# Optimization experiments

Hardware: AMD Instinct MI355X
Metric: run time of the kernel (lower is better)

Reference implementation:

```python
import jax, jax.numpy as jnp
import numpy as np

DIM = 256
NUM_HEADS = 8
HEAD_DIM = DIM // NUM_HEADS  # 32 (MQA: k/v projected to a single head)
RPE_DIM = 128
P = 10            # cpb table resolution per axis ('bilinear_4_10')
MAX_VALUE = 4.0
LOG_SCALE = 512.0
LOG2_8 = 3.0      # np.log2(8)


def _trilinear_sample(table, grid):
    """torch F.grid_sample 3D, mode='bilinear', padding_mode='zeros', align_corners=True.
    table: [C, D, H, W]; grid: [M, 3] with (x,y,z) in [-1,1] -> returns [C, M]."""
    C, D, H, W = table.shape
    x = (grid[:, 0] + 1.0) * 0.5 * (W - 1)
    y = (grid[:, 1] + 1.0) * 0.5 * (H - 1)
    z = (grid[:, 2] + 1.0) * 0.5 * (D - 1)
    x0f, y0f, z0f = jnp.floor(x), jnp.floor(y), jnp.floor(z)
    wx1, wy1, wz1 = x - x0f, y - y0f, z - z0f
    wx0, wy0, wz0 = 1.0 - wx1, 1.0 - wy1, 1.0 - wz1
    x0 = x0f.astype(jnp.int32); x1 = x0 + 1
    y0 = y0f.astype(jnp.int32); y1 = y0 + 1
    z0 = z0f.astype(jnp.int32); z1 = z0 + 1

    def corner(iz, iy, ix, w):
        inb = (iz >= 0) & (iz < D) & (iy >= 0) & (iy < H) & (ix >= 0) & (ix < W)
        v = table[:, jnp.clip(iz, 0, D - 1), jnp.clip(iy, 0, H - 1), jnp.clip(ix, 0, W - 1)]
        return v * jnp.where(inb, w, 0.0)[None, :]

    return (corner(z0, y0, x0, wz0 * wy0 * wx0) + corner(z0, y0, x1, wz0 * wy0 * wx1)
          + corner(z0, y1, x0, wz0 * wy1 * wx0) + corner(z0, y1, x1, wz0 * wy1 * wx1)
          + corner(z1, y0, x0, wz1 * wy0 * wx0) + corner(z1, y0, x1, wz1 * wy0 * wx1)
          + corner(z1, y1, x0, wz1 * wy1 * wx0) + corner(z1, y1, x1, wz1 * wy1 * wx1))


def setup_inputs() -> dict:
    rng = jax.random.key(0)
    ks = jax.random.split(rng, 12)
    B, nQ, nK = 2, 256, 2048
    s = 0.02
    return {
        "query": jax.random.normal(ks[0], (nQ, B, DIM), jnp.float32),
        "key": jax.random.normal(ks[1], (nK, B, DIM), jnp.float32),
        "reference_point": jax.random.normal(ks[2], (B, nQ, 8, 3), jnp.float32),
        "reference_angle": jax.random.normal(ks[3], (B, nQ), jnp.float32),
        "xyz_vol": jax.random.normal(ks[4], (B, nK, 3), jnp.float32),
        "q_w": jax.random.normal(ks[5], (DIM, DIM), jnp.float32) * s,
        "q_b": jnp.zeros((DIM,), jnp.float32),
        "k_w": jax.random.normal(ks[6], (DIM, HEAD_DIM), jnp.float32) * s,
        "k_b": jnp.zeros((HEAD_DIM,), jnp.float32),
        "v_w": jax.random.normal(ks[7], (DIM, HEAD_DIM), jnp.float32) * s,
        "v_b": jnp.zeros((HEAD_DIM,), jnp.float32),
        "proj_w": jax.random.normal(ks[8], (DIM, DIM), jnp.float32) * s,
        "proj_b": jnp.zeros((DIM,), jnp.float32),
        "cpb_w1": jax.random.normal(ks[9], (8, 3, RPE_DIM), jnp.float32) * s,
        "cpb_b1": jnp.zeros((8, RPE_DIM), jnp.float32),
        "cpb_w2": jax.random.normal(ks[10], (8, RPE_DIM, NUM_HEADS), jnp.float32) * s,
    }


def reference(query, key, reference_point, reference_angle, xyz_vol,
              q_w, q_b, k_w, k_b, v_w, v_b, proj_w, proj_b,
              cpb_w1, cpb_b1, cpb_w2):
    B, nQ = reference_point.shape[:2]
    nK = xyz_vol.shape[1]
    q_in = jnp.transpose(query, (1, 0, 2))  # [B, nQ, DIM]
    k_in = jnp.transpose(key, (1, 0, 2))    # [B, nK, DIM]

    # CPB MLP evaluated on the fixed coords table -> per-corner tables [8, NUM_HEADS, P, P, P]
    lin = jnp.linspace(-MAX_VALUE, MAX_VALUE, P, dtype=jnp.float32)
    coords = jnp.stack(jnp.meshgrid(lin, lin, lin, indexing='ij'), axis=-1)  # [P,P,P,3]
    hid = jax.nn.relu(jnp.einsum('pqrc,icd->ipqrd', coords, cpb_w1) + cpb_b1[:, None, None, None, :])
    tables = jnp.einsum('ipqrd,idh->ihpqr', hid, cpb_w2)

    # log-scaled relative deltas for all 8 corners (angle_type=='' -> no rotation branch)
    d = reference_point[:, :, None, :, :] - xyz_vol[:, None, :, None, :]  # [B,nQ,nK,8,3]
    d = jnp.sign(d) * jnp.log2(jnp.abs(d) * LOG_SCALE + 1.0) / LOG2_8 / MAX_VALUE
    grids = jnp.moveaxis(d, 3, 0).reshape(8, -1, 3)  # [8, B*nQ*nK, 3]

    sampled = jax.vmap(_trilinear_sample)(tables, grids)  # [8, NUM_HEADS, M]
    rpe = jnp.transpose(sampled.sum(0).reshape(NUM_HEADS, B, nQ, nK), (1, 0, 2, 3))  # [B,H,nQ,nK]

    scale = HEAD_DIM ** -0.5
    q = (q_in @ q_w + q_b).reshape(B, nQ, NUM_HEADS, HEAD_DIM)
    k = k_in @ k_w + k_b  # [B, nK, HEAD_DIM] (single shared KV head)
    v = k_in @ v_w + v_b
    attn = jnp.einsum('bqhd,bkd->bhqk', q * scale, k) + rpe
    attn = jax.nn.softmax(attn, axis=-1)
    x = jnp.einsum('bhqk,bkd->bqhd', attn, v).reshape(B, nQ, DIM)
    x = x @ proj_w + proj_b
    return jnp.transpose(x, (1, 0, 2)), attn
```

## Files before the change

kernel.cpp:

```cpp
#include <hip/hip_runtime.h>
#include <hip/hip_bf16.h>
#include <cstdint>

#define NQ 256
#define NK 2048
#define BB 2
#define SCALE 0.17677669529663687f

#define TB_OFF 0u
#define QP_OFF 128000u
#define KT_OFF 652288u
#define VP_OFF 1176576u

typedef unsigned short u16;
typedef _Float16 h16;
union U16x8 { uint4 u; h16 h[8]; };

__global__ __launch_bounds__(512) void k_prep(const float* __restrict__ query,
                                              const float* __restrict__ key,
                                              const float* __restrict__ qw,
                                              const float* __restrict__ qb,
                                              const float* __restrict__ kw,
                                              const float* __restrict__ kb,
                                              const float* __restrict__ vw,
                                              const float* __restrict__ vb,
                                              const float* __restrict__ w1g,
                                              const float* __restrict__ b1g,
                                              const float* __restrict__ w2g,
                                              u16* __restrict__ tb,
                                              float* __restrict__ qp,
                                              float* __restrict__ kpT,
                                              float* __restrict__ vp) {
  __shared__ __align__(16) char smraw[16 * 257 * 4];
  int bid = blockIdx.x, t = threadIdx.x;

  if (bid < 256) {
    float (*rows)[257] = (float(*)[257])smraw;
    int b = bid >> 7, kc = bid & 127;
    for (int idx = t; idx < 4096; idx += 512) {
      int r = idx >> 8, m = idx & 255;
      rows[r][m] = key[((kc * 16 + r) * BB + b) * 256 + m];
    }
    __syncthreads();
    int ks = t >> 5, d = t & 31;
    float a = kb[d], av = vb[d];
    #pragma unroll 4
    for (int m = 0; m < 256; ++m) {
      float rv = rows[ks][m];
      a  = fmaf(rv, kw[m * 32 + d], a);
      av = fmaf(rv, vw[m * 32 + d], av);
    }
    int k = kc * 16 + ks;
    vp[(b * NK + k) * 32 + d] = av;
    __syncthreads();
    float* f1 = (float*)smraw;
    f1[d * 16 + ks] = a;
    __syncthreads();
    int dd = t >> 4, kk = t & 15;
    kpT[(b * 32 + dd) * NK + kc * 16 + kk] = f1[dd * 16 + kk];
  } else if (bid < 320) {
    float (*rows)[257] = (float(*)[257])smraw;
    int qg = bid - 256;
    for (int idx = t; idx < 2048; idx += 512) {
      int r = idx >> 8, m = idx & 255;
      int g = qg * 8 + r, b = g >> 8, q = g & 255;
      rows[r][m] = query[(q * BB + b) * 256 + m];
    }
    __syncthreads();
    int r = t >> 6, c0 = (t & 63) * 4;
    int g = qg * 8 + r;
    float4 acc = *(const float4*)&qb[c0];
    #pragma unroll 4
    for (int m = 0; m < 256; ++m) {
      float rv = rows[r][m];
      float4 w4 = *(const float4*)&qw[m * 256 + c0];
      acc.x = fmaf(rv, w4.x, acc.x); acc.y = fmaf(rv, w4.y, acc.y);
      acc.z = fmaf(rv, w4.z, acc.z); acc.w = fmaf(rv, w4.w, acc.w);
    }
    float4 o; o.x = acc.x * SCALE; o.y = acc.y * SCALE; o.z = acc.z * SCALE; o.w = acc.w * SCALE;
    *(float4*)&qp[g * 256 + c0] = o;
  } else {
    float* w1 = (float*)smraw;
    float* b1 = w1 + 384;
    float* w2 = b1 + 128;
    int ib = bid - 320;
    int i = ib >> 2, cc = ib & 3;
    for (int idx = t; idx < 384; idx += 512) w1[idx] = w1g[i * 384 + idx];
    if (t < 128) b1[t] = b1g[i * 128 + t];
    for (int idx = t; idx < 1024; idx += 512) w2[idx] = w2g[i * 1024 + idx];
    __syncthreads();
    if (t < 250) {
      int cell = cc * 250 + t;
      int z = cell / 100, y = (cell / 10) % 10, x = cell % 10;
      const float step = 8.0f / 9.0f;
      float cz = -4.f + z * step, cy = -4.f + y * step, cx = -4.f + x * step;
      float o0 = 0, o1 = 0, o2 = 0, o3 = 0, o4 = 0, o5 = 0, o6 = 0, o7 = 0;
      for (int d = 0; d < 128; ++d) {
        float h = fmaxf(fmaf(cz, w1[d], fmaf(cy, w1[128 + d], fmaf(cx, w1[256 + d], b1[d]))), 0.f);
        const float* w2r = &w2[d * 8];
        o0 = fmaf(h, w2r[0], o0); o1 = fmaf(h, w2r[1], o1);
        o2 = fmaf(h, w2r[2], o2); o3 = fmaf(h, w2r[3], o3);
        o4 = fmaf(h, w2r[4], o4); o5 = fmaf(h, w2r[5], o5);
        o6 = fmaf(h, w2r[6], o6); o7 = fmaf(h, w2r[7], o7);
      }
      U16x8 R;
      R.h[0] = (h16)o0; R.h[1] = (h16)o1; R.h[2] = (h16)o2; R.h[3] = (h16)o3;
      R.h[4] = (h16)o4; R.h[5] = (h16)o5; R.h[6] = (h16)o6; R.h[7] = (h16)o7;
      *(uint4*)&tb[i * 8000 + cell * 8] = R.u;
    }
  }
}

struct Axis { int o0, o1; float w0, w1; };

static __device__ __forceinline__ Axis axis_setup(float dv, int stride) {
  float g = copysignf(__log2f(fmaf(fabsf(dv), 512.f, 1.f)) * (1.f / 12.f), dv);
  float p = fmaf(g, 4.5f, 4.5f);
  float f = floorf(p);
  int i0 = (int)f;
  float w1v = p - f;
  float w0v = 1.f - w1v;
  Axis a;
  a.w0 = ((unsigned)i0 <= 9u) ? w0v : 0.f;
  a.w1 = ((unsigned)(i0 + 1) <= 9u) ? w1v : 0.f;
  int c0 = min(max(i0, 0), 9);
  int c1 = min(max(i0 + 1, 0), 9);
  a.o0 = c0 * stride;
  a.o1 = c1 * stride;
  return a;
}

#define MIX2(A0, A1, U32, W) \
  asm("v_fma_mix_f32 %0, %1, %2, %0 op_sel:[0,0,0] op_sel_hi:[1,0,0]" : "+v"(A0) : "v"(U32), "v"(W)); \
  asm("v_fma_mix_f32 %0, %1, %2, %0 op_sel:[1,0,0] op_sel_hi:[1,0,0]" : "+v"(A1) : "v"(U32), "v"(W));

#define DO_CORNER(U, W, J) do { float ww = (W); \
  MIX2(acc[0][J], acc[1][J], (U).x, ww) \
  MIX2(acc[2][J], acc[3][J], (U).y, ww) \
  MIX2(acc[4][J], acc[5][J], (U).z, ww) \
  MIX2(acc[6][J], acc[7][J], (U).w, ww) } while (0)

__global__ __launch_bounds__(1024, 4) void k_mega(const u16* __restrict__ tbw,
                                                  const float* __restrict__ qp,
                                                  const float* __restrict__ kpT,
                                                  const float* __restrict__ xyz,
                                                  const float* __restrict__ refp,
                                                  const float* __restrict__ vp,
                                                  const float* __restrict__ pw,
                                                  const float* __restrict__ pb,
                                                  float* __restrict__ attn,
                                                  float* __restrict__ out) {
  __shared__ __align__(16) char un[131072];
  __shared__ __align__(16) float red4[2][8][8][32];
  __shared__ __align__(16) float qrow[2][256];
  __shared__ __align__(16) float rp[2][24];
  __shared__ __align__(16) float red[2][64];
  u16* tb = (u16*)un;
  float* p = (float*)un;

  int t = threadIdx.x;
  int b = blockIdx.x >> 7, qc = blockIdx.x & 127;
  for (int idx = t; idx < 8000; idx += 1024)
    ((uint4*)tb)[idx] = ((const uint4*)tbw)[idx];
  if (t < 128) {
    int qh2 = t >> 6, c = t & 63;
    ((float4*)qrow[qh2])[c] = ((const float4*)(qp + (b * 256 + qc * 2 + qh2) * 256))[c];
  } else if (t < 140) {
    int idx = t - 128;
    int qh2 = idx / 6, c = idx % 6;
    ((float4*)rp[qh2])[c] = ((const float4*)(refp + (b * 256 + qc * 2 + qh2) * 24))[c];
  }
  __syncthreads();

  int wv = t >> 6, l = t & 63;
  int qh = wv >> 3, wvl = wv & 7;
  int q = qc * 2 + qh;
  int k0 = wvl * 256 + l * 4;
  float acc[8][4] = {};

  const float* kT = kpT + b * (32 * NK);
  #pragma unroll 2
  for (int dq = 0; dq < 8; ++dq) {
    const float* kp0 = kT + (dq * 4) * NK + k0;
    float4 kv0 = *(const float4*)(kp0);
    float4 kv1 = *(const float4*)(kp0 + NK);
    float4 kv2 = *(const float4*)(kp0 + 2 * NK);
    float4 kv3 = *(const float4*)(kp0 + 3 * NK);
    #pragma unroll
    for (int h = 0; h < 8; ++h) {
      float4 qv = *(const float4*)&qrow[qh][h * 32 + dq * 4];
      acc[h][0] = fmaf(qv.x, kv0.x, fmaf(qv.y, kv1.x, fmaf(qv.z, kv2.x, fmaf(qv.w, kv3.x, acc[h][0]))));
      acc[h][1] = fmaf(qv.x, kv0.y, fmaf(qv.y, kv1.y, fmaf(qv.z, kv2.y, fmaf(qv.w, kv3.y, acc[h][1]))));
      acc[h][2] = fmaf(qv.x, kv0.z, fmaf(qv.y, kv1.z, fmaf(qv.z, kv2.z, fmaf(qv.w, kv3.z, acc[h][2]))));
      acc[h][3] = fmaf(qv.x, kv0.w, fmaf(qv.y, kv1.w, fmaf(qv.z, kv2.w, fmaf(qv.w, kv3.w, acc[h][3]))));
    }
  }

  {
    const float* xp = xyz + (size_t)(b * NK + k0) * 3;
    float4 X0 = *(const float4*)(xp);
    float4 X1 = *(const float4*)(xp + 4);
    float4 X2 = *(const float4*)(xp + 8);
    float xv[4] = { X0.x, X0.w, X1.z, X2.y };
    float yv[4] = { X0.y, X1.x, X1.w, X2.z };
    float zv[4] = { X0.z, X1.y, X2.x, X2.w };
    #pragma unroll 1
    for (int i = 0; i < 8; ++i) {
      float rx = rp[qh][i * 3 + 0];
      float ry = rp[qh][i * 3 + 1];
      float rz = rp[qh][i * 3 + 2];
      const u16* tp = tb + i * 8000;
      #pragma unroll
      for (int j = 0; j < 4; ++j) {
        Axis ax = axis_setup(rx - xv[j], 8);
        Axis ay = axis_setup(ry - yv[j], 80);
        Axis az = axis_setup(rz - zv[j], 800);
        int o00 = az.o0 + ay.o0, o01 = az.o0 + ay.o1;
        int o10 = az.o1 + ay.o0, o11 = az.o1 + ay.o1;
        float w00 = az.w0 * ay.w0, w01 = az.w0 * ay.w1;
        float w10 = az.w1 * ay.w0, w11 = az.w1 * ay.w1;
        uint4 u;
        u = *(const uint4*)(tp + o00 + ax.o0); DO_CORNER(u, w00 * ax.w0, j);
        u = *(const uint4*)(tp + o00 + ax.o1); DO_CORNER(u, w00 * ax.w1, j);
        u = *(const uint4*)(tp + o01 + ax.o0); DO_CORNER(u, w01 * ax.w0, j);
        u = *(const uint4*)(tp + o01 + ax.o1); DO_CORNER(u, w01 * ax.w1, j);
        u = *(const uint4*)(tp + o10 + ax.o0); DO_CORNER(u, w10 * ax.w0, j);
        u = *(const uint4*)(tp + o10 + ax.o1); DO_CORNER(u, w10 * ax.w1, j);
        u = *(const uint4*)(tp + o11 + ax.o0); DO_CORNER(u, w11 * ax.w0, j);
        u = *(const uint4*)(tp + o11 + ax.o1); DO_CORNER(u, w11 * ax.w1, j);
      }
    }
  }

  float mx[8];
  #pragma unroll
  for (int h = 0; h < 8; ++h) {
    float m = fmaxf(fmaxf(acc[h][0], acc[h][1]), fmaxf(acc[h][2], acc[h][3]));
    #pragma unroll
    for (int off = 32; off >= 1; off >>= 1) m = fmaxf(m, __shfl_xor(m, off, 64));
    mx[h] = m;
  }
  if (l == 0) {
    #pragma unroll
    for (int h = 0; h < 8; ++h) red[qh][h * 8 + wvl] = mx[h];
  }
  __syncthreads();
  #pragma unroll
  for (int h = 0; h < 8; ++h) {
    float4 r0 = *(const float4*)&red[qh][h * 8];
    float4 r1 = *(const float4*)&red[qh][h * 8 + 4];
    mx[h] = fmaxf(fmaxf(fmaxf(r0.x, r0.y), fmaxf(r0.z, r0.w)),
                  fmaxf(fmaxf(r1.x, r1.y), fmaxf(r1.z, r1.w)));
  }
  __syncthreads();
  float sm[8];
  #pragma unroll
  for (int h = 0; h < 8; ++h) {
    acc[h][0] = __expf(acc[h][0] - mx[h]);
    acc[h][1] = __expf(acc[h][1] - mx[h]);
    acc[h][2] = __expf(acc[h][2] - mx[h]);
    acc[h][3] = __expf(acc[h][3] - mx[h]);
    float s = (acc[h][0] + acc[h][1]) + (acc[h][2] + acc[h][3]);
    #pragma unroll
    for (int off = 32; off >= 1; off >>= 1) s += __shfl_xor(s, off, 64);
    sm[h] = s;
  }
  if (l == 0) {
    #pragma unroll
    for (int h = 0; h < 8; ++h) red[qh][h * 8 + wvl] = sm[h];
  }
  __syncthreads();
  #pragma unroll
  for (int h = 0; h < 8; ++h) {
    float4 r0 = *(const float4*)&red[qh][h * 8];
    float4 r1 = *(const float4*)&red[qh][h * 8 + 4];
    float s = ((r0.x + r0.y) + (r0.z + r0.w)) + ((r1.x + r1.y) + (r1.z + r1.w));
    float inv = 1.f / s;
    float4 pv;
    pv.x = acc[h][0] * inv; pv.y = acc[h][1] * inv;
    pv.z = acc[h][2] * inv; pv.w = acc[h][3] * inv;
    *(float4*)&p[(qh * 8 + h) * 2048 + k0] = pv;
    *(float4*)&attn[((size_t)((b * 8 + h) * 256 + q)) * 2048 + k0] = pv;
  }
  __syncthreads();

  {
    int ch = wv >> 1, pqh = wv & 1;
    int ks2 = l >> 3, dq = l & 7;
    float a2[8][4] = {};
    const float* vbase = vp + ((size_t)(b * NK + ch * 256)) * 32 + dq * 4;
    const float* prow = p + pqh * 16384 + ch * 256;
    #pragma unroll 2
    for (int kk = 0; kk < 32; ++kk) {
      int ko = kk * 8 + ks2;
      float4 v4 = *(const float4*)&vbase[ko * 32];
      #pragma unroll
      for (int h = 0; h < 8; ++h) {
        float pvv = prow[h * 2048 + ko];
        a2[h][0] = fmaf(pvv, v4.x, a2[h][0]);
        a2[h][1] = fmaf(pvv, v4.y, a2[h][1]);
        a2[h][2] = fmaf(pvv, v4.z, a2[h][2]);
        a2[h][3] = fmaf(pvv, v4.w, a2[h][3]);
      }
    }
    #pragma unroll
    for (int off = 8; off <= 32; off <<= 1) {
      #pragma unroll
      for (int h = 0; h < 8; ++h) {
        a2[h][0] += __shfl_xor(a2[h][0], off, 64);
        a2[h][1] += __shfl_xor(a2[h][1], off, 64);
        a2[h][2] += __shfl_xor(a2[h][2], off, 64);
        a2[h][3] += __shfl_xor(a2[h][3], off, 64);
      }
    }
    if (ks2 == 0) {
      #pragma unroll
      for (int h = 0; h < 8; ++h) {
        float4 w4; w4.x = a2[h][0]; w4.y = a2[h][1]; w4.z = a2[h][2]; w4.w = a2[h][3];
        *(float4*)&red4[pqh][ch][h][dq * 4] = w4;
      }
    }
  }
  __syncthreads();
  if (t < 512) {
    int pqh = t >> 8, m = t & 255;
    int h = m >> 5, d = m & 31;
    float s = 0.f;
    #pragma unroll
    for (int ch = 0; ch < 8; ++ch) s += red4[pqh][ch][h][d];
    qrow[pqh][m] = s;
  }
  __syncthreads();

  {
    float* scratch = (float*)red4;
    int c = t & 255, half = (t >> 8) & 1, pqh = t >> 9;
    int m0 = half * 128;
    float a = 0.f;
    #pragma unroll 4
    for (int m = 0; m < 128; ++m) {
      a = fmaf(qrow[pqh][m0 + m], pw[(m0 + m) * 256 + c], a);
    }
    scratch[(pqh * 2 + half) * 256 + c] = a;
  }
  __syncthreads();
  if (t < 512) {
    float* scratch = (float*)red4;
    int pqh = t >> 8, c = t & 255;
    float v = scratch[(pqh * 2) * 256 + c] + scratch[(pqh * 2 + 1) * 256 + c] + pb[c];
    int qq = qc * 2 + pqh;
    out[(qq * BB + b) * 256 + c] = v;
  }
}

extern "C" void kernel_launch(void* const* d_in, const int* in_sizes, int n_in,
                              void* d_out, int out_size, void* d_ws, size_t ws_size,
                              hipStream_t stream) {
  const float* query = (const float*)d_in[0];
  const float* key   = (const float*)d_in[1];
  const float* refp  = (const float*)d_in[2];
  const float* xyz   = (const float*)d_in[4];
  const float* qw    = (const float*)d_in[5];
  const float* qb    = (const float*)d_in[6];
  const float* kw    = (const float*)d_in[7];
  const float* kb    = (const float*)d_in[8];
  const float* vw    = (const float*)d_in[9];
  const float* vb    = (const float*)d_in[10];
  const float* pw    = (const float*)d_in[11];
  const float* pb    = (const float*)d_in[12];
  const float* w1    = (const float*)d_in[13];
  const float* b1    = (const float*)d_in[14];
  const float* w2    = (const float*)d_in[15];

  char* ws = (char*)d_ws;
  u16*   tb  = (u16*)(ws + TB_OFF);
  float* qp  = (float*)(ws + QP_OFF);
  float* kpT = (float*)(ws + KT_OFF);
  float* vp  = (float*)(ws + VP_OFF);
  float* out  = (float*)d_out;
  float* attn = out + 131072;

  hipLaunchKernelGGL(k_prep, dim3(352), dim3(512),  0, stream,
                     query, key, qw, qb, kw, kb, vw, vb, w1, b1, w2, tb, qp, kpT, vp);
  hipLaunchKernelGGL(k_mega, dim3(256), dim3(1024), 0, stream,
                     tb, qp, kpT, xyz, refp, vp, pw, pb, attn, out);
}
```

Before: 185.4 us.

## Split mega kernel to one query per block with two-pass table staging

Each block now handles one query instead of two, and the grid doubles to 512 blocks to fill more CUs. Shared memory is halved to 64KB, so the 8 CPB tables are loaded into LDS in two passes of four with extra barriers. Attention stores are coalesced through LDS, and the PV and projection stages are rebalanced to the single query. The cost is a second table load per block and more total table traffic, in exchange for better CU occupancy and parallelism.

```diff
diff --git a/kernel.cpp b/kernel.cpp
--- a/kernel.cpp
+++ b/kernel.cpp
@@ -140,7 +140,7 @@
   MIX2(acc[4][J], acc[5][J], (U).z, ww) \
   MIX2(acc[6][J], acc[7][J], (U).w, ww) } while (0)
 
-__global__ __launch_bounds__(1024, 4) void k_mega(const u16* __restrict__ tbw,
+__global__ __launch_bounds__(1024, 8) void k_mega(const u16* __restrict__ tbw,
                                                   const float* __restrict__ qp,
                                                   const float* __restrict__ kpT,
                                                   const float* __restrict__ xyz,
@@ -150,84 +150,82 @@
                                                   const float* __restrict__ pb,
                                                   float* __restrict__ attn,
                                                   float* __restrict__ out) {
-  __shared__ __align__(16) char un[131072];
-  __shared__ __align__(16) float red4[2][8][8][32];
-  __shared__ __align__(16) float qrow[2][256];
-  __shared__ __align__(16) float rp[2][24];
-  __shared__ __align__(16) float red[2][64];
+  __shared__ __align__(16) char un[65536];
+  __shared__ __align__(16) float red4[4][8][32];
+  __shared__ __align__(16) float qrow[256];
+  __shared__ __align__(16) float rp[24];
+  __shared__ __align__(16) float red[128];
   u16* tb = (u16*)un;
   float* p = (float*)un;
 
   int t = threadIdx.x;
-  int b = blockIdx.x >> 7, qc = blockIdx.x & 127;
-  for (int idx = t; idx < 8000; idx += 1024)
+  int b = blockIdx.x >> 8, q = blockIdx.x & 255;
+
+  for (int idx = t; idx < 4000; idx += 1024)
     ((uint4*)tb)[idx] = ((const uint4*)tbw)[idx];
-  if (t < 128) {
-    int qh2 = t >> 6, c = t & 63;
-    ((float4*)qrow[qh2])[c] = ((const float4*)(qp + (b * 256 + qc * 2 + qh2) * 256))[c];
-  } else if (t < 140) {
-    int idx = t - 128;
-    int qh2 = idx / 6, c = idx % 6;
-    ((float4*)rp[qh2])[c] = ((const float4*)(refp + (b * 256 + qc * 2 + qh2) * 24))[c];
-  }
+  if (t < 64) ((float4*)qrow)[t] = ((const float4*)(qp + (b * 256 + q) * 256))[t];
+  else if (t < 70) ((float4*)rp)[t - 64] = ((const float4*)(refp + (b * 256 + q) * 24))[t - 64];
   __syncthreads();
 
   int wv = t >> 6, l = t & 63;
-  int qh = wv >> 3, wvl = wv & 7;
-  int q = qc * 2 + qh;
-  int k0 = wvl * 256 + l * 4;
-  float acc[8][4] = {};
+  int k0 = wv * 128 + l * 2;
+  float acc[8][2] = {};
 
   const float* kT = kpT + b * (32 * NK);
   #pragma unroll 2
   for (int dq = 0; dq < 8; ++dq) {
     const float* kp0 = kT + (dq * 4) * NK + k0;
-    float4 kv0 = *(const float4*)(kp0);
-    float4 kv1 = *(const float4*)(kp0 + NK);
-    float4 kv2 = *(const float4*)(kp0 + 2 * NK);
-    float4 kv3 = *(const float4*)(kp0 + 3 * NK);
+    float2 kv0 = *(const float2*)(kp0);
+    float2 kv1 = *(const float2*)(kp0 + NK);
+    float2 kv2 = *(const float2*)(kp0 + 2 * NK);
+    float2 kv3 = *(const float2*)(kp0 + 3 * NK);
     #pragma unroll
     for (int h = 0; h < 8; ++h) {
-      float4 qv = *(const float4*)&qrow[qh][h * 32 + dq * 4];
+      float4 qv = *(const float4*)&qrow[h * 32 + dq * 4];
       acc[h][0] = fmaf(qv.x, kv0.x, fmaf(qv.y, kv1.x, fmaf(qv.z, kv2.x, fmaf(qv.w, kv3.x, acc[h][0]))));
       acc[h][1] = fmaf(qv.x, kv0.y, fmaf(qv.y, kv1.y, fmaf(qv.z, kv2.y, fmaf(qv.w, kv3.y, acc[h][1]))));
-      acc[h][2] = fmaf(qv.x, kv0.z, fmaf(qv.y, kv1.z, fmaf(qv.z, kv2.z, fmaf(qv.w, kv3.z, acc[h][2]))));
-      acc[h][3] = fmaf(qv.x, kv0.w, fmaf(qv.y, kv1.w, fmaf(qv.z, kv2.w, fmaf(qv.w, kv3.w, acc[h][3]))));
     }
   }
 
   {
     const float* xp = xyz + (size_t)(b * NK + k0) * 3;
-    float4 X0 = *(const float4*)(xp);
-    float4 X1 = *(const float4*)(xp + 4);
-    float4 X2 = *(const float4*)(xp + 8);
-    float xv[4] = { X0.x, X0.w, X1.z, X2.y };
-    float yv[4] = { X0.y, X1.x, X1.w, X2.z };
-    float zv[4] = { X0.z, X1.y, X2.x, X2.w };
+    float xv[2] = { xp[0], xp[3] };
+    float yv[2] = { xp[1], xp[4] };
+    float zv[2] = { xp[2], xp[5] };
     #pragma unroll 1
-    for (int i = 0; i < 8; ++i) {
-      float rx = rp[qh][i * 3 + 0];
-      float ry = rp[qh][i * 3 + 1];
-      float rz = rp[qh][i * 3 + 2];
-      const u16* tp = tb + i * 8000;
-      #pragma unroll
-      for (int j = 0; j < 4; ++j) {
-        Axis ax = axis_setup(rx - xv[j], 8);
-        Axis ay = axis_setup(ry - yv[j], 80);
-        Axis az = axis_setup(rz - zv[j], 800);
-        int o00 = az.o0 + ay.o0, o01 = az.o0 + ay.o1;
-        int o10 = az.o1 + ay.o0, o11 = az.o1 + ay.o1;
-        float w00 = az.w0 * ay.w0, w01 = az.w0 * ay.w1;
-        float w10 = az.w1 * ay.w0, w11 = az.w1 * ay.w1;
-        uint4 u;
-        u = *(const uint4*)(tp + o00 + ax.o0); DO_CORNER(u, w00 * ax.w0, j);
-        u = *(const uint4*)(tp + o00 + ax.o1); DO_CORNER(u, w00 * ax.w1, j);
-        u = *(const uint4*)(tp + o01 + ax.o0); DO_CORNER(u, w01 * ax.w0, j);
-        u = *(const uint4*)(tp + o01 + ax.o1); DO_CORNER(u, w01 * ax.w1, j);
-        u = *(const uint4*)(tp + o10 + ax.o0); DO_CORNER(u, w10 * ax.w0, j);
-        u = *(const uint4*)(tp + o10 + ax.o1); DO_CORNER(u, w10 * ax.w1, j);
-        u = *(const uint4*)(tp + o11 + ax.o0); DO_CORNER(u, w11 * ax.w0, j);
-        u = *(const uint4*)(tp + o11 + ax.o1); DO_CORNER(u, w11 * ax.w1, j);
+    for (int pass = 0; pass < 2; ++pass) {
+      if (pass) {
+        __syncthreads();
+        for (int idx = t; idx < 4000; idx += 1024)
+          ((uint4*)tb)[idx] = ((const uint4*)tbw)[4000 + idx];
+        __syncthreads();
+      }
+      #pragma unroll 1
+      for (int i4 = 0; i4 < 4; ++i4) {
+        int i = pass * 4 + i4;
+        float rx = rp[i * 3 + 0];
+        float ry = rp[i * 3 + 1];
+        float rz = rp[i * 3 + 2];
+        const u16* tp = tb + i4 * 8000;
+        #pragma unroll
+        for (int j = 0; j < 2; ++j) {
+          Axis ax = axis_setup(rx - xv[j], 8);
+          Axis ay = axis_setup(ry - yv[j], 80);
+          Axis az = axis_setup(rz - zv[j], 800);
+          int o00 = az.o0 + ay.o0, o01 = az.o0 + ay.o1;
+          int o10 = az.o1 + ay.o0, o11 = az.o1 + ay.o1;
+          float w00 = az.w0 * ay.w0, w01 = az.w0 * ay.w1;
+          float w10 = az.w1 * ay.w0, w11 = az.w1 * ay.w1;
+          uint4 u;
+          u = *(const uint4*)(tp + o00 + ax.o0); DO_CORNER(u, w00 * ax.w0, j);
+          u = *(const uint4*)(tp + o00 + ax.o1); DO_CORNER(u, w00 * ax.w1, j);
+          u = *(const uint4*)(tp + o01 + ax.o0); DO_CORNER(u, w01 * ax.w0, j);
+          u = *(const uint4*)(tp + o01 + ax.o1); DO_CORNER(u, w01 * ax.w1, j);
+          u = *(const uint4*)(tp + o10 + ax.o0); DO_CORNER(u, w10 * ax.w0, j);
+          u = *(const uint4*)(tp + o10 + ax.o1); DO_CORNER(u, w10 * ax.w1, j);
+          u = *(const uint4*)(tp + o11 + ax.o0); DO_CORNER(u, w11 * ax.w0, j);
+          u = *(const uint4*)(tp + o11 + ax.o1); DO_CORNER(u, w11 * ax.w1, j);
+        }
       }
     }
   }
@@ -235,121 +233,119 @@
   float mx[8];
   #pragma unroll
   for (int h = 0; h < 8; ++h) {
-    float m = fmaxf(fmaxf(acc[h][0], acc[h][1]), fmaxf(acc[h][2], acc[h][3]));
+    float m = fmaxf(acc[h][0], acc[h][1]);
     #pragma unroll
     for (int off = 32; off >= 1; off >>= 1) m = fmaxf(m, __shfl_xor(m, off, 64));
     mx[h] = m;
   }
   if (l == 0) {
     #pragma unroll
-    for (int h = 0; h < 8; ++h) red[qh][h * 8 + wvl] = mx[h];
+    for (int h = 0; h < 8; ++h) red[h * 16 + wv] = mx[h];
   }
   __syncthreads();
   #pragma unroll
   for (int h = 0; h < 8; ++h) {
-    float4 r0 = *(const float4*)&red[qh][h * 8];
-    float4 r1 = *(const float4*)&red[qh][h * 8 + 4];
-    mx[h] = fmaxf(fmaxf(fmaxf(r0.x, r0.y), fmaxf(r0.z, r0.w)),
-                  fmaxf(fmaxf(r1.x, r1.y), fmaxf(r1.z, r1.w)));
-  }
-  __syncthreads();
-  float sm[8];
+    float m = -1e30f;
+    #pragma unroll
+    for (int c4 = 0; c4 < 4; ++c4) {
+      float4 r4 = *(const float4*)&red[h * 16 + c4 * 4];
+      m = fmaxf(m, fmaxf(fmaxf(r4.x, r4.y), fmaxf(r4.z, r4.w)));
+    }
+    mx[h] = m;
+  }
+  __syncthreads();
   #pragma unroll
   for (int h = 0; h < 8; ++h) {
     acc[h][0] = __expf(acc[h][0] - mx[h]);
     acc[h][1] = __expf(acc[h][1] - mx[h]);
-    acc[h][2] = __expf(acc[h][2] - mx[h]);
-    acc[h][3] = __expf(acc[h][3] - mx[h]);
-    float s = (acc[h][0] + acc[h][1]) + (acc[h][2] + acc[h][3]);
+    float s = acc[h][0] + acc[h][1];
     #pragma unroll
     for (int off = 32; off >= 1; off >>= 1) s += __shfl_xor(s, off, 64);
-    sm[h] = s;
-  }
-  if (l == 0) {
-    #pragma unroll
-    for (int h = 0; h < 8; ++h) red[qh][h * 8 + wvl] = sm[h];
+    if (l == 0) red[h * 16 + wv] = s;
   }
   __syncthreads();
   #pragma unroll
   for (int h = 0; h < 8; ++h) {
-    float4 r0 = *(const float4*)&red[qh][h * 8];
-    float4 r1 = *(const float4*)&red[qh][h * 8 + 4];
-    float s = ((r0.x + r0.y) + (r0.z + r0.w)) + ((r1.x + r1.y) + (r1.z + r1.w));
+    float s = 0.f;
+    #pragma unroll
+    for (int c4 = 0; c4 < 4; ++c4) {
+      float4 r4 = *(const float4*)&red[h * 16 + c4 * 4];
+      s += (r4.x + r4.y) + (r4.z + r4.w);
+    }
     float inv = 1.f / s;
-    float4 pv;
+    float2 pv;
     pv.x = acc[h][0] * inv; pv.y = acc[h][1] * inv;
-    pv.z = acc[h][2] * inv; pv.w = acc[h][3] * inv;
-    *(float4*)&p[(qh * 8 + h) * 2048 + k0] = pv;
-    *(float4*)&attn[((size_t)((b * 8 + h) * 256 + q)) * 2048 + k0] = pv;
-  }
-  __syncthreads();
+    *(float2*)&p[h * 2048 + k0] = pv;
+  }
+  __syncthreads();
+
+  #pragma unroll
+  for (int c = 0; c < 4; ++c) {
+    int idx = c * 1024 + t;
+    int h = idx >> 9, kk4 = idx & 511;
+    *(float4*)&attn[((size_t)((b * 8 + h) * 256 + q)) * 2048 + kk4 * 4] = ((const float4*)p)[idx];
+  }
 
   {
-    int ch = wv >> 1, pqh = wv & 1;
+    int ch = wv >> 2, hh = wv & 3;
     int ks2 = l >> 3, dq = l & 7;
-    float a2[8][4] = {};
-    const float* vbase = vp + ((size_t)(b * NK + ch * 256)) * 32 + dq * 4;
-    const float* prow = p + pqh * 16384 + ch * 256;
+    float a2[2][4] = {};
+    const float* vbase = vp + ((size_t)(b * NK + ch * 512)) * 32 + dq * 4;
     #pragma unroll 2
     for (int kk = 0; kk < 32; ++kk) {
-      int ko = kk * 8 + ks2;
-      float4 v4 = *(const float4*)&vbase[ko * 32];
+      int krel = kk * 16 + ks2 * 2;
+      float4 v0 = *(const float4*)(vbase + (size_t)krel * 32);
+      float4 v1 = *(const float4*)(vbase + (size_t)(krel + 1) * 32);
       #pragma unroll
-      for (int h = 0; h < 8; ++h) {
-        float pvv = prow[h * 2048 + ko];
-        a2[h][0] = fmaf(pvv, v4.x, a2[h][0]);
-        a2[h][1] = fmaf(pvv, v4.y, a2[h][1]);
-        a2[h][2] = fmaf(pvv, v4.z, a2[h][2]);
-        a2[h][3] = fmaf(pvv, v4.w, a2[h][3]);
+      for (int ho = 0; ho < 2; ++ho) {
+        int h = hh * 2 + ho;
+        float2 pp = *(const float2*)&p[h * 2048 + ch * 512 + krel];
+        a2[ho][0] = fmaf(pp.x, v0.x, fmaf(pp.y, v1.x, a2[ho][0]));
+        a2[ho][1] = fmaf(pp.x, v0.y, fmaf(pp.y, v1.y, a2[ho][1]));
+        a2[ho][2] = fmaf(pp.x, v0.z, fmaf(pp.y, v1.z, a2[ho][2]));
+        a2[ho][3] = fmaf(pp.x, v0.w, fmaf(pp.y, v1.w, a2[ho][3]));
       }
     }
     #pragma unroll
     for (int off = 8; off <= 32; off <<= 1) {
       #pragma unroll
-      for (int h = 0; h < 8; ++h) {
-        a2[h][0] += __shfl_xor(a2[h][0], off, 64);
-        a2[h][1] += __shfl_xor(a2[h][1], off, 64);
-        a2[h][2] += __shfl_xor(a2[h][2], off, 64);
-        a2[h][3] += __shfl_xor(a2[h][3], off, 64);
+      for (int ho = 0; ho < 2; ++ho) {
+        a2[ho][0] += __shfl_xor(a2[ho][0], off, 64);
+        a2[ho][1] += __shfl_xor(a2[ho][1], off, 64);
+        a2[ho][2] += __shfl_xor(a2[ho][2], off, 64);
+        a2[ho][3] += __shfl_xor(a2[ho][3], off, 64);
       }
     }
     if (ks2 == 0) {
       #pragma unroll
-      for (int h = 0; h < 8; ++h) {
-        float4 w4; w4.x = a2[h][0]; w4.y = a2[h][1]; w4.z = a2[h][2]; w4.w = a2[h][3];
-        *(float4*)&red4[pqh][ch][h][dq * 4] = w4;
-      }
-    }
-  }
-  __syncthreads();
-  if (t < 512) {
-    int pqh = t >> 8, m = t & 255;
-    int h = m >> 5, d = m & 31;
-    float s = 0.f;
-    #pragma unroll
-    for (int ch = 0; ch < 8; ++ch) s += red4[pqh][ch][h][d];
-    qrow[pqh][m] = s;
+      for (int ho = 0; ho < 2; ++ho) {
+        float4 w4; w4.x = a2[ho][0]; w4.y = a2[ho][1]; w4.z = a2[ho][2]; w4.w = a2[ho][3];
+        *(float4*)&red4[ch][hh * 2 + ho][dq * 4] = w4;
+      }
+    }
+  }
+  __syncthreads();
+  if (t < 256) {
+    int h = t >> 5, d = t & 31;
+    qrow[t] = red4[0][h][d] + red4[1][h][d] + red4[2][h][d] + red4[3][h][d];
   }
   __syncthreads();
 
   {
     float* scratch = (float*)red4;
-    int c = t & 255, half = (t >> 8) & 1, pqh = t >> 9;
-    int m0 = half * 128;
+    int c = t & 255, q4 = t >> 8;
     float a = 0.f;
     #pragma unroll 4
-    for (int m = 0; m < 128; ++m) {
-      a = fmaf(qrow[pqh][m0 + m], pw[(m0 + m) * 256 + c], a);
-    }
-    scratch[(pqh * 2 + half) * 256 + c] = a;
-  }
-  __syncthreads();
-  if (t < 512) {
+    for (int m = 0; m < 64; ++m) {
+      a = fmaf(qrow[q4 * 64 + m], pw[(q4 * 64 + m) * 256 + c], a);
+    }
+    scratch[q4 * 256 + c] = a;
+  }
+  __syncthreads();
+  if (t < 256) {
     float* scratch = (float*)red4;
-    int pqh = t >> 8, c = t & 255;
-    float v = scratch[(pqh * 2) * 256 + c] + scratch[(pqh * 2 + 1) * 256 + c] + pb[c];
-    int qq = qc * 2 + pqh;
-    out[(qq * BB + b) * 256 + c] = v;
+    float v = scratch[t] + scratch[256 + t] + scratch[512 + t] + scratch[768 + t] + pb[t];
+    out[(q * BB + b) * 256 + t] = v;
   }
 }
 
@@ -382,6 +378,6 @@
 
   hipLaunchKernelGGL(k_prep, dim3(352), dim3(512),  0, stream,
                      query, key, qw, qb, kw, kb, vw, vb, w1, b1, w2, tb, qp, kpT, vp);
-  hipLaunchKernelGGL(k_mega, dim3(256), dim3(1024), 0, stream,
+  hipLaunchKernelGGL(k_mega, dim3(512), dim3(1024), 0, stream,
                      tb, qp, kpT, xyz, refp, vp, pw, pb, attn, out);
 }
```

Result: slower. 228.2 us (+23.0%).
